# Kernel tuning notes

Hardware: AMD Instinct MI355X
Metric: run time of the kernel (lower is better)

The kernel has to match this reference:

```python
import jax, jax.numpy as jnp
import numpy as np

HIDDEN = 1024
HEADS = 16
HEAD_DIM = HIDDEN // HEADS


def setup_inputs() -> dict:
    key = jax.random.key(0)
    ks = jax.random.split(key, 4)
    B, S, H = 2, 2048, HIDDEN
    scale = 1.0 / np.sqrt(H)
    return {
        "inputs": jax.random.normal(ks[0], (B, S, H), dtype=jnp.float32),
        "mask": jnp.ones((B, S), dtype=jnp.int32),
        "Wq": jax.random.normal(ks[1], (H, H), dtype=jnp.float32) * scale,
        "bq": jnp.zeros((H,), dtype=jnp.float32),
        "Wk": jax.random.normal(ks[2], (H, H), dtype=jnp.float32) * scale,
        "bk": jnp.zeros((H,), dtype=jnp.float32),
        "Wv": jax.random.normal(ks[3], (H, H), dtype=jnp.float32) * scale,
        "bv": jnp.zeros((H,), dtype=jnp.float32),
    }


def _split_heads(x, B, S):
    # [B,S,H] -> [B,heads,S,head_dim]
    return x.reshape(B, S, HEADS, HEAD_DIM).transpose(0, 2, 1, 3)


def reference(inputs, mask, Wq, bq, Wk, bk, Wv, bv):
    B, S, H = inputs.shape
    q = _split_heads(inputs @ Wq.T + bq, B, S)
    k = _split_heads(inputs @ Wk.T + bk, B, S)
    v = _split_heads(inputs @ Wv.T + bv, B, S)
    scores = jnp.einsum("bhqd,bhkd->bhqk", q, k) / jnp.sqrt(
        jnp.asarray(HEAD_DIM, dtype=inputs.dtype))
    # mask broadcast [B,1,1,S]; zeros -> -inf
    scores = jnp.where(mask[:, None, None, :] == 0, -jnp.inf, scores)
    attn = jax.nn.softmax(scores, axis=-1)
    context = jnp.einsum("bhqk,bhkd->bhqd", attn, v)
    return context.transpose(0, 2, 1, 3).reshape(B, S, H)
```

## Files before the change

kernel.cpp:

```cpp
#include <hip/hip_runtime.h>
#include <hip/hip_fp16.h>

constexpr int S_LEN  = 2048;
constexpr int HID    = 1024;
constexpr int HEADS  = 16;
constexpr int HDIM   = 64;
constexpr int BATCH  = 2;
constexpr int BH     = BATCH * HEADS;
constexpr int M_ROWS = BATCH * S_LEN;

typedef _Float16 half8  __attribute__((ext_vector_type(8)));
typedef _Float16 half4v __attribute__((ext_vector_type(4)));
typedef _Float16 half2v __attribute__((ext_vector_type(2)));
typedef float    f32x4  __attribute__((ext_vector_type(4)));

constexpr float EXP2_OFF = -11.541560327111707f;
constexpr float Q_SCALE  = 0.18033688011112042f;

__global__ __launch_bounds__(256) void cvt_kernel(
    const float* __restrict__ X,  const float* __restrict__ Wq,
    const float* __restrict__ Wk, const float* __restrict__ Wv,
    const int* __restrict__ mask,
    _Float16* __restrict__ Xh,  _Float16* __restrict__ Wqh,
    _Float16* __restrict__ Wkh, _Float16* __restrict__ Wvh,
    float* __restrict__ maskF)
{
    const int blk = blockIdx.x;
    if (blk >= 3584) {
        const int loc = blk - 3584;
        const size_t e = ((size_t)loc * 256 + threadIdx.x) * 8;
        #pragma unroll
        for (int i = 0; i < 8; ++i)
            maskF[e + i] = mask[e + i] ? EXP2_OFF : -1.0e30f;
        return;
    }
    const float* src; _Float16* dst; int loc;
    if (blk < 2048)      { src = X;  dst = Xh;  loc = blk; }
    else if (blk < 2560) { src = Wq; dst = Wqh; loc = blk - 2048; }
    else if (blk < 3072) { src = Wk; dst = Wkh; loc = blk - 2560; }
    else                 { src = Wv; dst = Wvh; loc = blk - 3072; }
    const size_t e = ((size_t)loc * 256 + threadIdx.x) * 8;
    float4 a = *reinterpret_cast<const float4*>(&src[e]);
    float4 b = *reinterpret_cast<const float4*>(&src[e + 4]);
    half8 h = { (_Float16)a.x, (_Float16)a.y, (_Float16)a.z, (_Float16)a.w,
                (_Float16)b.x, (_Float16)b.y, (_Float16)b.z, (_Float16)b.w };
    *reinterpret_cast<half8*>(&dst[e]) = h;
}

__device__ __forceinline__ void async_cp16(_Float16* lds, const _Float16* g) {
    __builtin_amdgcn_global_load_lds(
        (const __attribute__((address_space(1))) void*)g,
        (__attribute__((address_space(3))) void*)lds, 16, 0, 0);
}

__global__ __launch_bounds__(256) void qkv_proj_kernel(
    const _Float16* __restrict__ Xh,
    const _Float16* __restrict__ Wqh, const _Float16* __restrict__ Wkh,
    const _Float16* __restrict__ Wvh,
    const float* __restrict__ bq, const float* __restrict__ bk,
    const float* __restrict__ bv,
    _Float16* __restrict__ Qo, _Float16* __restrict__ Ko,
    _Float16* __restrict__ Vo)
{
    const int mode = blockIdx.z;
    const _Float16* W    = (mode == 0) ? Wqh : (mode == 1) ? Wkh : Wvh;
    const float*    bias = (mode == 0) ? bq  : (mode == 1) ? bk  : bv;
    _Float16*       Out  = (mode == 0) ? Qo  : (mode == 1) ? Ko  : Vo;

    const int m0 = blockIdx.x * 128, n0 = blockIdx.y * 128;
    const int tid = threadIdx.x, wave = tid >> 6, lane = tid & 63;
    const int l15 = lane & 15, quad = lane >> 4;

    __shared__ _Float16 As[128 * 64];
    __shared__ _Float16 Bs[128 * 64];

    f32x4 acc[4][4];
    #pragma unroll
    for (int mt = 0; mt < 4; ++mt)
        #pragma unroll
        for (int nt = 0; nt < 4; ++nt) acc[mt][nt] = (f32x4){0.f, 0.f, 0.f, 0.f};

    const int wm = (wave & 1) * 64, wn = (wave >> 1) * 64;

    for (int k0 = 0; k0 < HID; k0 += 64) {
        #pragma unroll
        for (int i = 0; i < 4; ++i) {
            const int chunk = wave * 4 + i;
            const int row   = chunk * 8 + (lane >> 3);
            const int lofs  = chunk * 512 + lane * 8;
            const int scol  = (lane & 7) * 8;
            async_cp16(&As[lofs], &Xh[(size_t)(m0 + row) * HID + k0 + scol]);
            async_cp16(&Bs[lofs], &W [(size_t)(n0 + row) * HID + k0 + scol]);
        }
        __syncthreads();

        #pragma unroll
        for (int c = 0; c < 2; ++c) {
            half8 af[4], bf[4];
            #pragma unroll
            for (int mt = 0; mt < 4; ++mt)
                af[mt] = *reinterpret_cast<const half8*>(
                    &As[(wm + mt * 16 + l15) * 64 + c * 32 + quad * 8]);
            #pragma unroll
            for (int nt = 0; nt < 4; ++nt)
                bf[nt] = *reinterpret_cast<const half8*>(
                    &Bs[(wn + nt * 16 + l15) * 64 + c * 32 + quad * 8]);
            #pragma unroll
            for (int mt = 0; mt < 4; ++mt)
                #pragma unroll
                for (int nt = 0; nt < 4; ++nt)
                    acc[mt][nt] = __builtin_amdgcn_mfma_f32_16x16x32_f16(
                        af[mt], bf[nt], acc[mt][nt], 0, 0, 0);
        }
        __syncthreads();
    }

    #pragma unroll
    for (int nt = 0; nt < 4; ++nt) {
        const int n = n0 + wn + nt * 16 + l15;
        const float bias_n = bias[n];
        const int h = n >> 6, d = n & 63;
        #pragma unroll
        for (int mt = 0; mt < 4; ++mt) {
            #pragma unroll
            for (int r = 0; r < 4; ++r) {
                const int m = m0 + wm + mt * 16 + quad * 4 + r;
                const int b = m >> 11, s = m & 2047;
                const int bh = b * HEADS + h;
                float v = acc[mt][nt][r] + bias_n;
                if (mode == 0) v *= Q_SCALE;
                Out[((size_t)bh * S_LEN + s) * HDIM + d] = (_Float16)v;
            }
        }
    }
}

__global__ __launch_bounds__(256) void vtrans_kernel(
    const _Float16* __restrict__ V, _Float16* __restrict__ Vt)
{
    __shared__ _Float16 T[64][72];
    const int bh = blockIdx.y, s0 = blockIdx.x * 64, tid = threadIdx.x;

    const _Float16* src = V + ((size_t)bh * S_LEN + s0) * HDIM;
    #pragma unroll
    for (int i = 0; i < 2; ++i) {
        const int slot = tid + i * 256;
        const int row = slot >> 3, c8 = (slot & 7) * 8;
        half8 v = *reinterpret_cast<const half8*>(&src[row * HDIM + c8]);
        #pragma unroll
        for (int j = 0; j < 8; ++j) T[c8 + j][row] = v[j];
    }
    __syncthreads();

    _Float16* dst = Vt + (size_t)bh * HDIM * S_LEN + s0;
    #pragma unroll
    for (int i = 0; i < 2; ++i) {
        const int slot = tid + i * 256;
        const int d = slot >> 3, s8 = (slot & 7) * 8;
        half8 v = *reinterpret_cast<const half8*>(&T[d][s8]);
        *reinterpret_cast<half8*>(&dst[(size_t)d * S_LEN + s8]) = v;
    }
}

__global__ __launch_bounds__(512) void attn_kernel(
    const _Float16* __restrict__ Q, const _Float16* __restrict__ K,
    const _Float16* __restrict__ Vt, const float* __restrict__ maskF,
    float* __restrict__ Out)
{
    const int id    = blockIdx.x;
    const int xcd   = id & 7, local = id >> 3;
    const int bh    = xcd * 4 + (local & 3);
    const int qt    = local >> 2;
    const int b = bh >> 4, h = bh & 15;
    const int tid = threadIdx.x, wave = tid >> 6, lane = tid & 63;
    const int l15 = lane & 15, quad = lane >> 4;

    __shared__ _Float16 Ks[2][64 * 64];
    __shared__ _Float16 Vs[2][64 * 64];
    __shared__ _Float16 Ps[8][16][68];

    const _Float16* Qb = Q  + (size_t)bh * S_LEN * HDIM;
    const _Float16* Kb = K  + (size_t)bh * S_LEN * HDIM;
    const _Float16* Vb = Vt + (size_t)bh * HDIM * S_LEN;
    const float*    mb = maskF + b * S_LEN;

    const int qrow = qt * 128 + wave * 16 + l15;
    half8 qf[2];
    qf[0] = *reinterpret_cast<const half8*>(&Qb[(size_t)qrow * HDIM + quad * 8]);
    qf[1] = *reinterpret_cast<const half8*>(&Qb[(size_t)qrow * HDIM + 32 + quad * 8]);

    f32x4 acc[4];
    #pragma unroll
    for (int mt = 0; mt < 4; ++mt) acc[mt] = (f32x4){0.f, 0.f, 0.f, 0.f};
    float den = 0.f;

    const int srow_t  = tid >> 3;
    const int schunk  = (tid & 7) ^ (srow_t & 7);
    auto stage = [&](int kb, int buf) {
        async_cp16(&Ks[buf][tid * 8],
                   &Kb[(size_t)(kb + srow_t) * HDIM + schunk * 8]);
        async_cp16(&Vs[buf][tid * 8],
                   &Vb[(size_t)srow_t * S_LEN + kb + schunk * 8]);
    };

    stage(0, 0);
    int buf = 0;
    const int rsw = (l15 & 7);

    for (int kb = 0; kb < S_LEN; kb += 64) {
        __syncthreads();
        if (kb + 64 < S_LEN) stage(kb + 64, buf ^ 1);

        float4 m4[4];
        #pragma unroll
        for (int nt = 0; nt < 4; ++nt)
            m4[nt] = *reinterpret_cast<const float4*>(&mb[kb + nt * 16 + quad * 4]);

        half8 kf[2][4];
        #pragma unroll
        for (int c = 0; c < 2; ++c)
            #pragma unroll
            for (int nt = 0; nt < 4; ++nt)
                kf[c][nt] = *reinterpret_cast<const half8*>(
                    &Ks[buf][(nt * 16 + l15) * 64 + ((c * 4 + quad) ^ rsw) * 8]);
        f32x4 sc[4];
        #pragma unroll
        for (int nt = 0; nt < 4; ++nt) sc[nt] = (f32x4){0.f, 0.f, 0.f, 0.f};
        #pragma unroll
        for (int c = 0; c < 2; ++c)
            #pragma unroll
            for (int nt = 0; nt < 4; ++nt)
                sc[nt] = __builtin_amdgcn_mfma_f32_16x16x32_f16(
                    kf[c][nt], qf[c], sc[nt], 0, 0, 0);

        half8 vf[2][4];
        #pragma unroll
        for (int c = 0; c < 2; ++c)
            #pragma unroll
            for (int mt = 0; mt < 4; ++mt)
                vf[c][mt] = *reinterpret_cast<const half8*>(
                    &Vs[buf][(mt * 16 + l15) * 64 + ((c * 4 + quad) ^ rsw) * 8]);

        #pragma unroll
        for (int nt = 0; nt < 4; ++nt) {
            float p0 = __builtin_amdgcn_exp2f(sc[nt][0] + m4[nt].x);
            float p1 = __builtin_amdgcn_exp2f(sc[nt][1] + m4[nt].y);
            float p2 = __builtin_amdgcn_exp2f(sc[nt][2] + m4[nt].z);
            float p3 = __builtin_amdgcn_exp2f(sc[nt][3] + m4[nt].w);
            den += (p0 + p1) + (p2 + p3);
            half2v lo = __builtin_bit_cast(half2v, __builtin_amdgcn_cvt_pkrtz(p0, p1));
            half2v hi = __builtin_bit_cast(half2v, __builtin_amdgcn_cvt_pkrtz(p2, p3));
            half4v pk = { lo[0], lo[1], hi[0], hi[1] };
            *reinterpret_cast<half4v*>(&Ps[wave][l15][nt * 16 + quad * 4]) = pk;
        }
        asm volatile("s_waitcnt lgkmcnt(0)" ::: "memory");

        #pragma unroll
        for (int c = 0; c < 2; ++c) {
            half4v plo = *reinterpret_cast<const half4v*>(
                &Ps[wave][l15][c * 32 + quad * 8]);
            half4v phi = *reinterpret_cast<const half4v*>(
                &Ps[wave][l15][c * 32 + quad * 8 + 4]);
            half8 pf = { plo[0], plo[1], plo[2], plo[3],
                         phi[0], phi[1], phi[2], phi[3] };
            #pragma unroll
            for (int mt = 0; mt < 4; ++mt)
                acc[mt] = __builtin_amdgcn_mfma_f32_16x16x32_f16(
                    vf[c][mt], pf, acc[mt], 0, 0, 0);
        }
        buf ^= 1;
    }

    den += __shfl_xor(den, 16, 64);
    den += __shfl_xor(den, 32, 64);
    const float inv = 1.0f / den;

    float* orow = Out + ((size_t)(b * S_LEN + qrow)) * HID + h * HDIM;
    #pragma unroll
    for (int mt = 0; mt < 4; ++mt) {
        float4 o = { acc[mt][0] * inv, acc[mt][1] * inv,
                     acc[mt][2] * inv, acc[mt][3] * inv };
        *reinterpret_cast<float4*>(&orow[mt * 16 + quad * 4]) = o;
    }
}

extern "C" void kernel_launch(void* const* d_in, const int* in_sizes, int n_in,
                              void* d_out, int out_size, void* d_ws, size_t ws_size,
                              hipStream_t stream) {
    const float* X  = (const float*)d_in[0];
    const int*   mk = (const int*)  d_in[1];
    const float* Wq = (const float*)d_in[2];
    const float* bq = (const float*)d_in[3];
    const float* Wk = (const float*)d_in[4];
    const float* bk = (const float*)d_in[5];
    const float* Wv = (const float*)d_in[6];
    const float* bv = (const float*)d_in[7];
    float* out = (float*)d_out;

    _Float16* XhVt = (_Float16*)d_ws;
    _Float16* Wqh  = XhVt + (size_t)M_ROWS * HID;
    _Float16* Wkh  = Wqh + (size_t)HID * HID;
    _Float16* Wvh  = Wkh + (size_t)HID * HID;
    _Float16* Q    = Wvh + (size_t)HID * HID;
    _Float16* K    = Q   + (size_t)BH * S_LEN * HDIM;
    _Float16* Vo   = K   + (size_t)BH * S_LEN * HDIM;
    float*    maskF = (float*)(Vo + (size_t)BH * S_LEN * HDIM);

    cvt_kernel<<<3586, 256, 0, stream>>>(X, Wq, Wk, Wv, mk, XhVt, Wqh, Wkh, Wvh, maskF);

    dim3 gp(M_ROWS / 128, HID / 128, 3);
    qkv_proj_kernel<<<gp, 256, 0, stream>>>(XhVt, Wqh, Wkh, Wvh, bq, bk, bv, Q, K, Vo);

    dim3 gt(S_LEN / 64, BH);
    vtrans_kernel<<<gt, 256, 0, stream>>>(Vo, XhVt);

    attn_kernel<<<512, 512, 0, stream>>>(Q, K, XhVt, maskF, out);
}
```

Before: 189.8 us.

## Fuse V transpose into QKV projection epilogue via LDS-staged coalesced stores

Removes the separate vtrans kernel by having the projection epilogue write V directly in transposed [bh][d][s] layout. Each wave stages its 64x64 output tile in padded LDS, then emits 16-byte coalesced global stores for Q, K and Vt instead of scattered 2-byte stores. This drops one kernel launch and a full read/write pass over V. In exchange it adds a larger shared buffer that reuses the A/B tile space, and relies on a wave-local lgkmcnt wait for correctness.

Result: faster. 182.7 us (-3.7%).

```diff
diff --git a/kernel.cpp b/kernel.cpp
--- a/kernel.cpp
+++ b/kernel.cpp
@@ -60,19 +60,19 @@
     const float* __restrict__ bq, const float* __restrict__ bk,
     const float* __restrict__ bv,
     _Float16* __restrict__ Qo, _Float16* __restrict__ Ko,
-    _Float16* __restrict__ Vo)
+    _Float16* __restrict__ Vt)
 {
     const int mode = blockIdx.z;
     const _Float16* W    = (mode == 0) ? Wqh : (mode == 1) ? Wkh : Wvh;
     const float*    bias = (mode == 0) ? bq  : (mode == 1) ? bk  : bv;
-    _Float16*       Out  = (mode == 0) ? Qo  : (mode == 1) ? Ko  : Vo;
 
     const int m0 = blockIdx.x * 128, n0 = blockIdx.y * 128;
     const int tid = threadIdx.x, wave = tid >> 6, lane = tid & 63;
     const int l15 = lane & 15, quad = lane >> 4;
 
-    __shared__ _Float16 As[128 * 64];
-    __shared__ _Float16 Bs[128 * 64];
+    __shared__ _Float16 SMEM[18432];
+    _Float16* As = SMEM;
+    _Float16* Bs = SMEM + 8192;
 
     f32x4 acc[4][4];
     #pragma unroll
@@ -114,51 +114,61 @@
         }
         __syncthreads();
     }
-
-    #pragma unroll
-    for (int nt = 0; nt < 4; ++nt) {
-        const int n = n0 + wn + nt * 16 + l15;
-        const float bias_n = bias[n];
-        const int h = n >> 6, d = n & 63;
-        #pragma unroll
-        for (int mt = 0; mt < 4; ++mt) {
-            #pragma unroll
-            for (int r = 0; r < 4; ++r) {
-                const int m = m0 + wm + mt * 16 + quad * 4 + r;
-                const int b = m >> 11, s = m & 2047;
-                const int bh = b * HEADS + h;
-                float v = acc[mt][nt][r] + bias_n;
-                if (mode == 0) v *= Q_SCALE;
-                Out[((size_t)bh * S_LEN + s) * HDIM + d] = (_Float16)v;
+    _Float16* T = SMEM + wave * 4608;
+
+    const int nn  = n0 + wn;
+    const int hh  = nn >> 6;
+    const int mm  = m0 + wm;
+    const int bb  = mm >> 11;
+    const int bhv = bb * HEADS + hh;
+    const int s0  = mm & 2047;
+    const int rowg = lane >> 3, chunk = lane & 7;
+
+    if (mode < 2) {
+        _Float16* Out = (mode == 0) ? Qo : Ko;
+        #pragma unroll
+        for (int nt = 0; nt < 4; ++nt) {
+            const int col = nt * 16 + l15;
+            float bias_n = bias[nn + col];
+            #pragma unroll
+            for (int mt = 0; mt < 4; ++mt)
+                #pragma unroll
+                for (int r = 0; r < 4; ++r) {
+                    float v = acc[mt][nt][r] + bias_n;
+                    if (mode == 0) v *= Q_SCALE;
+                    T[(mt * 16 + quad * 4 + r) * 72 + col] = (_Float16)v;
+                }
+        }
+        asm volatile("s_waitcnt lgkmcnt(0)" ::: "memory");
+        #pragma unroll
+        for (int j = 0; j < 8; ++j) {
+            const int srow = j * 8 + rowg;
+            half8 v = *reinterpret_cast<const half8*>(&T[srow * 72 + chunk * 8]);
+            *reinterpret_cast<half8*>(
+                &Out[((size_t)bhv * S_LEN + s0 + srow) * HDIM + chunk * 8]) = v;
+        }
+    } else {
+        #pragma unroll
+        for (int nt = 0; nt < 4; ++nt) {
+            const int col = nt * 16 + l15;
+            const float bias_n = bias[nn + col];
+            #pragma unroll
+            for (int mt = 0; mt < 4; ++mt) {
+                half4v t = { (_Float16)(acc[mt][nt][0] + bias_n),
+                             (_Float16)(acc[mt][nt][1] + bias_n),
+                             (_Float16)(acc[mt][nt][2] + bias_n),
+                             (_Float16)(acc[mt][nt][3] + bias_n) };
+                *reinterpret_cast<half4v*>(&T[col * 72 + mt * 16 + quad * 4]) = t;
             }
         }
-    }
-}
-
-__global__ __launch_bounds__(256) void vtrans_kernel(
-    const _Float16* __restrict__ V, _Float16* __restrict__ Vt)
-{
-    __shared__ _Float16 T[64][72];
-    const int bh = blockIdx.y, s0 = blockIdx.x * 64, tid = threadIdx.x;
-
-    const _Float16* src = V + ((size_t)bh * S_LEN + s0) * HDIM;
-    #pragma unroll
-    for (int i = 0; i < 2; ++i) {
-        const int slot = tid + i * 256;
-        const int row = slot >> 3, c8 = (slot & 7) * 8;
-        half8 v = *reinterpret_cast<const half8*>(&src[row * HDIM + c8]);
-        #pragma unroll
-        for (int j = 0; j < 8; ++j) T[c8 + j][row] = v[j];
-    }
-    __syncthreads();
-
-    _Float16* dst = Vt + (size_t)bh * HDIM * S_LEN + s0;
-    #pragma unroll
-    for (int i = 0; i < 2; ++i) {
-        const int slot = tid + i * 256;
-        const int d = slot >> 3, s8 = (slot & 7) * 8;
-        half8 v = *reinterpret_cast<const half8*>(&T[d][s8]);
-        *reinterpret_cast<half8*>(&dst[(size_t)d * S_LEN + s8]) = v;
+        asm volatile("s_waitcnt lgkmcnt(0)" ::: "memory");
+        #pragma unroll
+        for (int j = 0; j < 8; ++j) {
+            const int drow = j * 8 + rowg;
+            half8 v = *reinterpret_cast<const half8*>(&T[drow * 72 + chunk * 8]);
+            *reinterpret_cast<half8*>(
+                &Vt[((size_t)bhv * HDIM + drow) * S_LEN + s0 + chunk * 8]) = v;
+        }
     }
 }
 
@@ -297,22 +307,19 @@
     const float* bv = (const float*)d_in[7];
     float* out = (float*)d_out;
 
-    _Float16* XhVt = (_Float16*)d_ws;
-    _Float16* Wqh  = XhVt + (size_t)M_ROWS * HID;
-    _Float16* Wkh  = Wqh + (size_t)HID * HID;
-    _Float16* Wvh  = Wkh + (size_t)HID * HID;
-    _Float16* Q    = Wvh + (size_t)HID * HID;
-    _Float16* K    = Q   + (size_t)BH * S_LEN * HDIM;
-    _Float16* Vo   = K   + (size_t)BH * S_LEN * HDIM;
-    float*    maskF = (float*)(Vo + (size_t)BH * S_LEN * HDIM);
-
-    cvt_kernel<<<3586, 256, 0, stream>>>(X, Wq, Wk, Wv, mk, XhVt, Wqh, Wkh, Wvh, maskF);
+    _Float16* Xh  = (_Float16*)d_ws;
+    _Float16* Wqh = Xh  + (size_t)M_ROWS * HID;
+    _Float16* Wkh = Wqh + (size_t)HID * HID;
+    _Float16* Wvh = Wkh + (size_t)HID * HID;
+    _Float16* Q   = Wvh + (size_t)HID * HID;
+    _Float16* K   = Q   + (size_t)BH * S_LEN * HDIM;
+    _Float16* Vt  = K   + (size_t)BH * S_LEN * HDIM;
+    float*    maskF = (float*)(Vt + (size_t)BH * S_LEN * HDIM);
+
+    cvt_kernel<<<3586, 256, 0, stream>>>(X, Wq, Wk, Wv, mk, Xh, Wqh, Wkh, Wvh, maskF);
 
     dim3 gp(M_ROWS / 128, HID / 128, 3);
-    qkv_proj_kernel<<<gp, 256, 0, stream>>>(XhVt, Wqh, Wkh, Wvh, bq, bk, bv, Q, K, Vo);
-
-    dim3 gt(S_LEN / 64, BH);
-    vtrans_kernel<<<gt, 256, 0, stream>>>(Vo, XhVt);
-
-    attn_kernel<<<512, 512, 0, stream>>>(Q, K, XhVt, maskF, out);
-}
+    qkv_proj_kernel<<<gp, 256, 0, stream>>>(Xh, Wqh, Wkh, Wvh, bq, bk, bv, Q, K, Vt);
+
+    attn_kernel<<<512, 512, 0, stream>>>(Q, K, Vt, maskF, out);
+}
```
